# Kernel tuning notes

Measured on AMD Instinct MI355X. Metric: run time of the kernel, lower is better.

## Reference

```python
import jax, jax.numpy as jnp
import numpy as np

N_NODES = 20000
N_EDGES = 320000
N_RELS = 500
EMB = 256
D4 = EMB // 4
B = 32
GAMMA = 12.0
BN_EPS = 1e-5


def _linear(x, W, b):
    return x @ W.T + b


def _bn(x, g, b, m, v):
    # BatchNorm1d in eval mode with running stats
    return (x - m) * jax.lax.rsqrt(v + BN_EPS) * g + b


def _comp_layer(src, dst, h, e, WO, bO, WI, bI, WS, bS, bng, bnb, bnm, bnv):
    # CompGCNLayer: u_sub_e message + per-node mean over in-edges ('ho')
    # and, on the reversed graph, over out-edges ('hi'); nodes with no
    # incident edges get 0 (dgl mean semantics).
    n = h.shape[0]
    ones = jnp.ones(src.shape[0], h.dtype)
    deg_in = jnp.maximum(jax.ops.segment_sum(ones, dst, num_segments=n), 1.0)
    deg_out = jnp.maximum(jax.ops.segment_sum(ones, src, num_segments=n), 1.0)
    ho = jax.ops.segment_sum(h[src] - e, dst, num_segments=n) / deg_in[:, None]
    hi = jax.ops.segment_sum(h[dst] - e, src, num_segments=n) / deg_out[:, None]
    out = (_linear(ho, WO, bO) + _linear(hi, WI, bI) + _linear(h, WS, bS)) / 3.0
    return _bn(out, bng, bnb, bnm, bnv)


def _forward(node_embs, edge_embs, params, src, dst, e_vid, hids, rids, tids,
             is_update_g_embs, is_head_pred):
    (W_O1, b_O1, W_I1, b_I1, W_S1, b_S1, bn1_g, bn1_b, bn1_m, bn1_v, Wr1, br1,
     W_O2, b_O2, W_I2, b_I2, W_S2, b_S2, bn2_g, bn2_b, bn2_m, bn2_v, Wr2, br2) = params
    if is_update_g_embs:
        he = edge_embs[e_vid]                                   # [E, D]
        h1 = jnp.tanh(_comp_layer(src, dst, node_embs, he,
                                  W_O1, b_O1, W_I1, b_I1, W_S1, b_S1,
                                  bn1_g, bn1_b, bn1_m, bn1_v))  # [N, D/4]
        he1 = jnp.tanh(_linear(he, Wr1, br1))                   # [E, D/4]
        hn = jnp.tanh(_comp_layer(src, dst, h1, he1,
                                  W_O2, b_O2, W_I2, b_I2, W_S2, b_S2,
                                  bn2_g, bn2_b, bn2_m, bn2_v))  # [N, D]
    else:
        hn = node_embs
    heads = hn[hids]
    tails = hn[tids]
    rels = _linear(jax.nn.relu(_linear(edge_embs[rids], Wr1, br1)), Wr2, br2)
    b = hids.shape[0]
    n = hn.shape[0]
    # Faithful to torch repeat_interleave indexing in predict():
    # flat element k pairs query row k//C with candidate row k//B.
    cand_idx = (jnp.arange(b)[:, None] * n + jnp.arange(n)[None, :]) // b  # [B, N]
    cand = hn[cand_idx]                                                    # [B, N, D]
    if is_head_pred == 1:
        diff = cand + (rels - tails)[:, None, :]
    else:
        diff = (heads + rels)[:, None, :] - cand
    dist = jnp.sqrt(jnp.sum(diff * diff, axis=-1))  # p = norm = 2
    score = jax.nn.sigmoid(GAMMA - dist)
    return hn, score


def setup_inputs() -> dict:
    key = jax.random.key(0)
    ks = jax.random.split(key, 20)
    w = lambda k, shp: jax.random.normal(k, shp, jnp.float32) * 0.05
    inp = {
        "node_embs": jax.random.normal(ks[0], (N_NODES, EMB), jnp.float32),
        "edge_embs": jax.random.normal(ks[1], (N_RELS, EMB), jnp.float32),
        "W_O1": w(ks[2], (D4, EMB)), "b_O1": jnp.zeros((D4,), jnp.float32),
        "W_I1": w(ks[3], (D4, EMB)), "b_I1": jnp.zeros((D4,), jnp.float32),
        "W_S1": w(ks[4], (D4, EMB)), "b_S1": jnp.zeros((D4,), jnp.float32),
        "bn1_g": jnp.ones((D4,), jnp.float32), "bn1_b": jnp.zeros((D4,), jnp.float32),
        "bn1_m": jnp.zeros((D4,), jnp.float32), "bn1_v": jnp.ones((D4,), jnp.float32),
        "Wr1": w(ks[5], (D4, EMB)), "br1": jnp.zeros((D4,), jnp.float32),
        "W_O2": w(ks[6], (EMB, D4)), "b_O2": jnp.zeros((EMB,), jnp.float32),
        "W_I2": w(ks[7], (EMB, D4)), "b_I2": jnp.zeros((EMB,), jnp.float32),
        "W_S2": w(ks[8], (EMB, D4)), "b_S2": jnp.zeros((EMB,), jnp.float32),
        "bn2_g": jnp.ones((EMB,), jnp.float32), "bn2_b": jnp.zeros((EMB,), jnp.float32),
        "bn2_m": jnp.zeros((EMB,), jnp.float32), "bn2_v": jnp.ones((EMB,), jnp.float32),
        "Wr2": w(ks[9], (EMB, D4)), "br2": jnp.zeros((EMB,), jnp.float32),
        "src": jax.random.randint(ks[10], (N_EDGES,), 0, N_NODES, jnp.int32),
        "dst": jax.random.randint(ks[11], (N_EDGES,), 0, N_NODES, jnp.int32),
        "e_vid": jax.random.randint(ks[12], (N_EDGES,), 0, N_RELS, jnp.int32),
        "hids": jax.random.randint(ks[13], (B,), 0, N_NODES, jnp.int32),
        "rids": jax.random.randint(ks[14], (B,), 0, N_RELS, jnp.int32),
        "tids": jax.random.randint(ks[15], (B,), 0, N_NODES, jnp.int32),
        "is_update_g_embs": 1,
        "is_head_pred": 0,
    }
    return inp


def reference(node_embs, edge_embs,
              W_O1, b_O1, W_I1, b_I1, W_S1, b_S1, bn1_g, bn1_b, bn1_m, bn1_v,
              Wr1, br1,
              W_O2, b_O2, W_I2, b_I2, W_S2, b_S2, bn2_g, bn2_b, bn2_m, bn2_v,
              Wr2, br2,
              src, dst, e_vid, hids, rids, tids,
              is_update_g_embs, is_head_pred):
    params = (W_O1, b_O1, W_I1, b_I1, W_S1, b_S1, bn1_g, bn1_b, bn1_m, bn1_v,
              Wr1, br1,
              W_O2, b_O2, W_I2, b_I2, W_S2, b_S2, bn2_g, bn2_b, bn2_m, bn2_v,
              Wr2, br2)
    return _forward(node_embs, edge_embs, params, src, dst, e_vid,
                    hids, rids, tids, is_update_g_embs, is_head_pred)
```

## Files before the change

kernel.cpp:

```cpp
#include <hip/hip_runtime.h>
#include <math.h>

#define NN 20000
#define NE 320000
#define NR 500
#define EMBD 256
#define D4 64
#define BQ 32
#define TOT (2 * NN)
#define NB 40

#define NBLK_HIST 1250
#define NBLK_BN 448
#define NBLK_K1 (NBLK_HIST + NBLK_BN + 2)

#define NBLK_GC1 939
#define NBLK_GE1 32
#define NBLK_MEGA (NBLK_GC1 + NBLK_GE1 + NBLK_HIST)

typedef __attribute__((ext_vector_type(8))) short bf16x8;
typedef __attribute__((ext_vector_type(4))) float f32x4;

__device__ __forceinline__ unsigned short f2bf(float x)
{
    unsigned int u = __float_as_uint(x);
    unsigned int r = (u + 0x7fffu + ((u >> 16) & 1u)) >> 16;
    return (unsigned short)r;
}

__global__ __launch_bounds__(256) void k_prep(
    const int* __restrict__ src, const int* __restrict__ dst, int* __restrict__ cnt,
    const float* __restrict__ W_O1, const float* __restrict__ W_I1,
    const float* __restrict__ W_S1, const float* __restrict__ Wr1,
    const float* __restrict__ W_O2, const float* __restrict__ W_I2,
    const float* __restrict__ W_S2,
    unsigned short* __restrict__ Bn1, unsigned short* __restrict__ Bn2,
    const float* __restrict__ bO1, const float* __restrict__ bI1,
    const float* __restrict__ bS1,
    const float* __restrict__ g1, const float* __restrict__ bb1,
    const float* __restrict__ m1, const float* __restrict__ v1,
    const float* __restrict__ bO2, const float* __restrict__ bI2,
    const float* __restrict__ bS2,
    const float* __restrict__ g2, const float* __restrict__ bb2,
    const float* __restrict__ m2, const float* __restrict__ v2,
    float* __restrict__ s1, float* __restrict__ t1,
    float* __restrict__ s2, float* __restrict__ t2)
{
    int b = blockIdx.x;
    if (b < NBLK_HIST) {
        int i = b * 256 + threadIdx.x;
        if (i < NE) {
            atomicAdd(&cnt[dst[i]], 1);
            atomicAdd(&cnt[NN + src[i]], 1);
        }
        return;
    }
    b -= NBLK_HIST;
    if (b >= NBLK_BN) {
        int i = (b - NBLK_BN) * 256 + threadIdx.x;
        if (i < 64) {
            float rsg = g1[i] / sqrtf(v1[i] + 1e-5f);
            s1[i] = rsg * (1.f / 3.f);
            t1[i] = ((bO1[i] + bI1[i] + bS1[i]) * (1.f / 3.f) - m1[i]) * rsg + bb1[i];
        } else if (i < 320) {
            int n = i - 64;
            float rsg = g2[n] / sqrtf(v2[n] + 1e-5f);
            s2[n] = rsg * (1.f / 3.f);
            t2[n] = ((bO2[n] + bI2[n] + bS2[n]) * (1.f / 3.f) - m2[n]) * rsg + bb2[n];
        }
        return;
    }
    int id = b * 256 + threadIdx.x;
    if (id < 256 * 256) {
        int n = id >> 8, k = id & 255;
        float v;
        if (n < 64)       v = W_O1[n * 256 + k];
        else if (n < 128) v = W_I1[(n - 64) * 256 + k];
        else if (n < 192) v = W_S1[(n - 128) * 256 + k];
        else              v = Wr1[(n - 192) * 256 + k];
        Bn1[id] = f2bf(v);
    } else {
        int id2 = id - 256 * 256;
        if (id2 < 256 * 192) {
            int n = id2 / 192, k = id2 - n * 192;
            float v;
            if (k < 64)       v = W_O2[n * 64 + k];
            else if (k < 128) v = W_I2[n * 64 + (k - 64)];
            else              v = W_S2[n * 64 + (k - 128)];
            Bn2[id2] = f2bf(v);
        }
    }
}


__global__ __launch_bounds__(256) void k_scanA(const int* __restrict__ cnt,
                                               int* __restrict__ bsum)
{
    __shared__ int lds[256];
    int t = threadIdx.x;
    int base = blockIdx.x * 1024 + t * 4;
    int s = 0;
    if (base + 3 < TOT) {
        int4 v = *(const int4*)(cnt + base);
        s = v.x + v.y + v.z + v.w;
    } else {
        for (int c = 0; c < 4; ++c) { int i = base + c; if (i < TOT) s += cnt[i]; }
    }
    lds[t] = s;
    __syncthreads();
    for (int d = 128; d > 0; d >>= 1) {
        if (t < d) lds[t] += lds[t + d];
        __syncthreads();
    }
    if (t == 0) bsum[blockIdx.x] = lds[0];
}

__global__ __launch_bounds__(64) void k_scanB(int* __restrict__ bsum)
{
    int t = threadIdx.x;
    int v = (t < NB) ? bsum[t] : 0;
#pragma unroll
    for (int d = 1; d < 64; d <<= 1) {
        int u = __shfl_up(v, d, 64);
        if (t >= d) v += u;
    }
    int ex = __shfl_up(v, 1, 64);
    if (t == 0) ex = 0;
    if (t < NB) bsum[t] = ex;
}

__global__ __launch_bounds__(256) void k_scanC(const int* __restrict__ cnt,
                                               const int* __restrict__ bsum,
                                               int* __restrict__ offc,
                                               int* __restrict__ cur)
{
    __shared__ int lds[256];
    int t = threadIdx.x;
    int base = blockIdx.x * 1024 + t * 4;
    int e0 = 0, e1 = 0, e2 = 0, e3 = 0;
    if (base + 3 < TOT) {
        int4 v = *(const int4*)(cnt + base);
        e0 = v.x; e1 = v.y; e2 = v.z; e3 = v.w;
    } else {
        if (base + 0 < TOT) e0 = cnt[base + 0];
        if (base + 1 < TOT) e1 = cnt[base + 1];
        if (base + 2 < TOT) e2 = cnt[base + 2];
        if (base + 3 < TOT) e3 = cnt[base + 3];
    }
    int s = e0 + e1 + e2 + e3;
    lds[t] = s;
    __syncthreads();
    for (int d = 1; d < 256; d <<= 1) {
        int u = (t >= d) ? lds[t - d] : 0;
        __syncthreads();
        lds[t] += u;
        __syncthreads();
    }
    int run = lds[t] - s + bsum[blockIdx.x];
    if (base + 3 < TOT) {
        int4 o = make_int4(run, run + e0, run + e0 + e1, run + e0 + e1 + e2);
        *(int4*)(offc + base) = o;
        *(int4*)(cur + base) = o;
    } else {
        int r = run;
        if (base + 0 < TOT) { offc[base + 0] = r; cur[base + 0] = r; r += e0; }
        if (base + 1 < TOT) { offc[base + 1] = r; cur[base + 1] = r; r += e1; }
        if (base + 2 < TOT) { offc[base + 2] = r; cur[base + 2] = r; r += e2; }
        if (base + 3 < TOT) { offc[base + 3] = r; cur[base + 3] = r; r += e3; }
    }
    if (blockIdx.x == 0 && t == 0) offc[TOT] = 2 * NE;
}

__device__ __forceinline__ void gemm_dev(
    unsigned short* As, unsigned short* Bs,
    const float* __restrict__ A, int M, int K, int lda,
    const unsigned short* __restrict__ Bn,
    float* __restrict__ C, int ldc, int mode,
    const float* __restrict__ sv, const float* __restrict__ tv,
    const float* __restrict__ node_embs, const int* __restrict__ flag,
    int m0, int n0)
{
    const int t = threadIdx.x;
    const int lane = t & 63, wave = t >> 6;
    const int wr = wave >> 1, wc = wave & 1;
    const int lrow = lane & 15, lkg = lane >> 4;

    f32x4 acc[2][2] = {};

    for (int kb = 0; kb < K; kb += 64) {
#pragma unroll
        for (int it = 0; it < 4; ++it) {
            int idx = t + it * 256;
            int kq = idx & 15;
            int row = idx >> 4;
            int gm = m0 + row;
            float4 a = make_float4(0.f, 0.f, 0.f, 0.f);
            if (gm < M) a = *(const float4*)(A + (size_t)gm * lda + kb + 4 * kq);
            unsigned int p0 = (unsigned int)f2bf(a.x) | ((unsigned int)f2bf(a.y) << 16);
            unsigned int p1 = (unsigned int)f2bf(a.z) | ((unsigned int)f2bf(a.w) << 16);
            *(uint2*)&As[row * 72 + 4 * kq] = make_uint2(p0, p1);
        }
#pragma unroll
        for (int it = 0; it < 2; ++it) {
            int idx = t + it * 256;
            int ko = idx & 7;
            int row = idx >> 3;
            uint4 b = *(const uint4*)(Bn + (size_t)(n0 + row) * K + kb + 8 * ko);
            *(uint4*)&Bs[row * 72 + 8 * ko] = b;
        }
        __syncthreads();
#pragma unroll
        for (int ks = 0; ks < 2; ++ks) {
            int k0 = ks * 32 + lkg * 8;
            bf16x8 af0 = *(const bf16x8*)&As[(wr * 32 + lrow) * 72 + k0];
            bf16x8 af1 = *(const bf16x8*)&As[(wr * 32 + 16 + lrow) * 72 + k0];
            bf16x8 bf0 = *(const bf16x8*)&Bs[(wc * 32 + lrow) * 72 + k0];
            bf16x8 bf1 = *(const bf16x8*)&Bs[(wc * 32 + 16 + lrow) * 72 + k0];
            acc[0][0] = __builtin_amdgcn_mfma_f32_16x16x32_bf16(af0, bf0, acc[0][0], 0, 0, 0);
            acc[0][1] = __builtin_amdgcn_mfma_f32_16x16x32_bf16(af0, bf1, acc[0][1], 0, 0, 0);
            acc[1][0] = __builtin_amdgcn_mfma_f32_16x16x32_bf16(af1, bf0, acc[1][0], 0, 0, 0);
            acc[1][1] = __builtin_amdgcn_mfma_f32_16x16x32_bf16(af1, bf1, acc[1][1], 0, 0, 0);
        }
        __syncthreads();
    }

#pragma unroll
    for (int m = 0; m < 2; ++m) {
#pragma unroll
        for (int r = 0; r < 4; ++r) {
            int gm = m0 + wr * 32 + m * 16 + lkg * 4 + r;
            if (gm >= M) continue;
#pragma unroll
            for (int n = 0; n < 2; ++n) {
                int gn = n0 + wc * 32 + n * 16 + lrow;
                float v = acc[m][n][r];
                if (mode == 0) {
                    C[(size_t)gm * ldc + gn] = v;
                } else if (mode == 1) {
                    float val = (gn >= 192) ? tanhf(v + sv[gn - 192]) : v;
                    C[(size_t)gm * ldc + gn] = val;
                } else {
                    float val = tanhf(v * sv[gn] + tv[gn]);
                    if (flag[0] == 0) val = node_embs[(size_t)gm * EMBD + gn];
                    C[(size_t)gm * EMBD + gn] = val;
                }
            }
        }
    }
}

__global__ __launch_bounds__(256) void gemm_mfma(
    const float* __restrict__ A, int M, int K, int lda,
    const unsigned short* __restrict__ Bn,
    float* __restrict__ C, int ldc, int mode,
    const float* __restrict__ sv, const float* __restrict__ tv,
    const float* __restrict__ node_embs, const int* __restrict__ flag)
{
    __shared__ unsigned short As[64 * 72];
    __shared__ unsigned short Bs[64 * 72];
    gemm_dev(As, Bs, A, M, K, lda, Bn, C, ldc, mode, sv, tv, node_embs, flag,
             blockIdx.x * 64, blockIdx.y * 64);
}

__global__ __launch_bounds__(256) void k_mega(
    const float* __restrict__ node_embs, const float* __restrict__ edge_embs,
    const unsigned short* __restrict__ Bn1,
    float* __restrict__ C1, float* __restrict__ E1, const float* __restrict__ br1,
    const int* __restrict__ src, const int* __restrict__ dst,
    const int* __restrict__ evid,
    int* __restrict__ cur, unsigned* __restrict__ R)
{
    __shared__ unsigned short As[64 * 72];
    __shared__ unsigned short Bs[64 * 72];
    int bid = blockIdx.x;
    if (bid < NBLK_GC1) {
        gemm_dev(As, Bs, node_embs, NN, 256, 256, Bn1, C1, 192, 0,
                 nullptr, nullptr, nullptr, nullptr,
                 (bid % 313) * 64, (bid / 313) * 64);
    } else if (bid < NBLK_GC1 + NBLK_GE1) {
        int b2 = bid - NBLK_GC1;
        gemm_dev(As, Bs, edge_embs, NR, 256, 256, Bn1, E1, 256, 1,
                 br1, nullptr, nullptr, nullptr,
                 (b2 % 8) * 64, (b2 / 8) * 64);
    } else {
        int e = (bid - NBLK_GC1 - NBLK_GE1) * 256 + threadIdx.x;
        if (e < NE) {
            int s = src[e], d = dst[e];
            unsigned rv = (unsigned)evid[e] << 15;
            int p = atomicAdd(&cur[d], 1);
            R[p] = (unsigned)s | rv;
            int q = atomicAdd(&cur[NN + s], 1);
            R[q] = (unsigned)d | rv;
        }
    }
}


__device__ __forceinline__ void gather_quad(
    const unsigned* __restrict__ R, int r0, int r1, int g, int q,
    const float* __restrict__ TAB, int ldt, int toff,
    const float* __restrict__ ETAB, int eoff,
    float4& acc)
{
    int lane = g * 16 + q;
    int cnt = r1 - r0;
    for (int base = 0; base < cnt; base += 64) {
        int rem = cnt - base; if (rem > 64) rem = 64;
        unsigned rec = 0u;
        if (lane < rem) rec = R[r0 + base + lane];
        int i = 0;
        for (; 4 * i + 15 < rem; i += 4) {
            unsigned ra = __shfl(rec, 4 * i + g, 64);
            unsigned rb = __shfl(rec, 4 * i + 4 + g, 64);
            unsigned rc = __shfl(rec, 4 * i + 8 + g, 64);
            unsigned rd = __shfl(rec, 4 * i + 12 + g, 64);
            float4 a0 = *(const float4*)(TAB + (size_t)(ra & 0x7FFFu) * ldt + toff + 4 * q);
            float4 e0 = *(const float4*)(ETAB + (size_t)(ra >> 15) * 256 + eoff + 4 * q);
            float4 a1 = *(const float4*)(TAB + (size_t)(rb & 0x7FFFu) * ldt + toff + 4 * q);
            float4 e1 = *(const float4*)(ETAB + (size_t)(rb >> 15) * 256 + eoff + 4 * q);
            float4 a2 = *(const float4*)(TAB + (size_t)(rc & 0x7FFFu) * ldt + toff + 4 * q);
            float4 e2 = *(const float4*)(ETAB + (size_t)(rc >> 15) * 256 + eoff + 4 * q);
            float4 a3 = *(const float4*)(TAB + (size_t)(rd & 0x7FFFu) * ldt + toff + 4 * q);
            float4 e3 = *(const float4*)(ETAB + (size_t)(rd >> 15) * 256 + eoff + 4 * q);
            acc.x += (a0.x - e0.x) + (a1.x - e1.x) + (a2.x - e2.x) + (a3.x - e3.x);
            acc.y += (a0.y - e0.y) + (a1.y - e1.y) + (a2.y - e2.y) + (a3.y - e3.y);
            acc.z += (a0.z - e0.z) + (a1.z - e1.z) + (a2.z - e2.z) + (a3.z - e3.z);
            acc.w += (a0.w - e0.w) + (a1.w - e1.w) + (a2.w - e2.w) + (a3.w - e3.w);
        }
        for (; 4 * i < rem; ++i) {
            int idx = 4 * i + g;
            unsigned rr = __shfl(rec, idx < rem ? idx : 0, 64);
            if (idx < rem) {
                float4 a = *(const float4*)(TAB + (size_t)(rr & 0x7FFFu) * ldt + toff + 4 * q);
                float4 e = *(const float4*)(ETAB + (size_t)(rr >> 15) * 256 + eoff + 4 * q);
                acc.x += a.x - e.x; acc.y += a.y - e.y;
                acc.z += a.z - e.z; acc.w += a.w - e.w;
            }
        }
    }
}

__device__ __forceinline__ void xreduce(float4& v)
{
    v.x += __shfl_xor(v.x, 16, 64); v.y += __shfl_xor(v.y, 16, 64);
    v.z += __shfl_xor(v.z, 16, 64); v.w += __shfl_xor(v.w, 16, 64);
    v.x += __shfl_xor(v.x, 32, 64); v.y += __shfl_xor(v.y, 32, 64);
    v.z += __shfl_xor(v.z, 32, 64); v.w += __shfl_xor(v.w, 32, 64);
}

__global__ __launch_bounds__(256) void k_gather1(
    const int* __restrict__ offc, const unsigned* __restrict__ R,
    const float* __restrict__ C1, const float* __restrict__ E1,
    const float* __restrict__ s1, const float* __restrict__ t1,
    float* __restrict__ A2)
{
    int n = blockIdx.x * 4 + (threadIdx.x >> 6);
    if (n >= NN) return;
    int lane = threadIdx.x & 63, g = lane >> 4, q = lane & 15;
    int b0 = offc[n], b1 = offc[n + 1];
    int c0 = offc[NN + n], c1 = offc[NN + n + 1];
    float di = 1.f / fmaxf((float)(b1 - b0), 1.f);
    float dh = 1.f / fmaxf((float)(c1 - c0), 1.f);
    float4 accO = make_float4(0.f, 0.f, 0.f, 0.f);
    float4 accI = make_float4(0.f, 0.f, 0.f, 0.f);
    gather_quad(R, b0, b1, g, q, C1, 192, 0, E1, 0, accO);
    gather_quad(R, c0, c1, g, q, C1, 192, 64, E1, 64, accI);
    xreduce(accO);
    xreduce(accI);
    if (g == 0) {
        float4 hs = *(const float4*)(C1 + (size_t)n * 192 + 128 + 4 * q);
        float4 sv = *(const float4*)(s1 + 4 * q);
        float4 tv = *(const float4*)(t1 + 4 * q);
        float4 o;
        o.x = tanhf((accO.x * di + accI.x * dh + hs.x) * sv.x + tv.x);
        o.y = tanhf((accO.y * di + accI.y * dh + hs.y) * sv.y + tv.y);
        o.z = tanhf((accO.z * di + accI.z * dh + hs.z) * sv.z + tv.z);
        o.w = tanhf((accO.w * di + accI.w * dh + hs.w) * sv.w + tv.w);
        *(float4*)(A2 + (size_t)n * 192 + 128 + 4 * q) = o;
    }
}

__global__ __launch_bounds__(256) void k_gather2(
    const int* __restrict__ offc, const unsigned* __restrict__ R,
    const float* __restrict__ A2r, const float* __restrict__ E1,
    float* __restrict__ A2w)
{
    int n = blockIdx.x * 4 + (threadIdx.x >> 6);
    if (n >= NN) return;
    int lane = threadIdx.x & 63, g = lane >> 4, q = lane & 15;
    int b0 = offc[n], b1 = offc[n + 1];
    int c0 = offc[NN + n], c1 = offc[NN + n + 1];
    float di = 1.f / fmaxf((float)(b1 - b0), 1.f);
    float dh = 1.f / fmaxf((float)(c1 - c0), 1.f);
    float4 accO = make_float4(0.f, 0.f, 0.f, 0.f);
    float4 accI = make_float4(0.f, 0.f, 0.f, 0.f);
    gather_quad(R, b0, b1, g, q, A2r, 192, 128, E1, 192, accO);
    gather_quad(R, c0, c1, g, q, A2r, 192, 128, E1, 192, accI);
    xreduce(accO);
    xreduce(accI);
    if (g == 0) {
        float4 o0, o1;
        o0.x = accO.x * di; o0.y = accO.y * di; o0.z = accO.z * di; o0.w = accO.w * di;
        o1.x = accI.x * dh; o1.y = accI.y * dh; o1.z = accI.z * dh; o1.w = accI.w * dh;
        *(float4*)(A2w + (size_t)n * 192 + 4 * q) = o0;
        *(float4*)(A2w + (size_t)n * 192 + 64 + 4 * q) = o1;
    }
}

__global__ __launch_bounds__(64) void k_rels(
    const float* __restrict__ edge_embs,
    const float* __restrict__ Wr1, const float* __restrict__ br1,
    const float* __restrict__ Wr2, const float* __restrict__ br2,
    const int* __restrict__ hids, const int* __restrict__ rids, const int* __restrict__ tids,
    const int* __restrict__ is_head, const float* __restrict__ hn,
    float* __restrict__ tvec)
{
    __shared__ float e_s[256];
    __shared__ float m_s[64];
    int b = blockIdx.x, o = threadIdx.x;
    int rid = rids[b];
#pragma unroll
    for (int q = 0; q < 4; ++q) e_s[o + 64 * q] = edge_embs[(size_t)rid * 256 + o + 64 * q];
    __syncthreads();
    float acc = br1[o];
    for (int k = 0; k < 256; ++k) acc = fmaf(e_s[k], Wr1[o * 256 + k], acc);
    m_s[o] = fmaxf(acc, 0.f);
    __syncthreads();
    int ih = is_head[0];
    int nid = ih ? tids[b] : hids[b];
#pragma unroll
    for (int q = 0; q < 4; ++q) {
        int n = o + 64 * q;
        float r = br2[n];
        for (int jj = 0; jj < 64; ++jj) r = fmaf(m_s[jj], Wr2[n * 64 + jj], r);
        float hv = hn[(size_t)nid * 256 + n];
        tvec[b * 256 + n] = ih ? (hv - r) : (hv + r);
    }
}

__global__ __launch_bounds__(256) void k_score(
    const float* __restrict__ hn, const float* __restrict__ tvec,
    float* __restrict__ score)
{
    int p = blockIdx.x * 4 + (threadIdx.x >> 6);
    if (p >= BQ * (NN / BQ)) return;
    int l = threadIdx.x & 63;
    int b = p / (NN / BQ);
    int j = p - b * (NN / BQ);
    int idx = (b * NN + 32 * j) / BQ;
    float ssum = 0.f;
#pragma unroll
    for (int q = 0; q < 4; ++q) {
        float df = hn[(size_t)idx * 256 + l + 64 * q] - tvec[b * 256 + l + 64 * q];
        ssum = fmaf(df, df, ssum);
    }
#pragma unroll
    for (int off = 32; off >= 1; off >>= 1) ssum += __shfl_xor(ssum, off, 64);
    float dist = sqrtf(ssum);
    float sc = 1.f / (1.f + expf(dist - 12.f));
    if (l < 32) score[(size_t)b * NN + 32 * j + l] = sc;
}

extern "C" void kernel_launch(void* const* d_in, const int* in_sizes, int n_in,
                              void* d_out, int out_size, void* d_ws, size_t ws_size,
                              hipStream_t stream)
{
    const float* node_embs = (const float*)d_in[0];
    const float* edge_embs = (const float*)d_in[1];
    const float* W_O1 = (const float*)d_in[2];  const float* b_O1 = (const float*)d_in[3];
    const float* W_I1 = (const float*)d_in[4];  const float* b_I1 = (const float*)d_in[5];
    const float* W_S1 = (const float*)d_in[6];  const float* b_S1 = (const float*)d_in[7];
    const float* bn1_g = (const float*)d_in[8]; const float* bn1_b = (const float*)d_in[9];
    const float* bn1_m = (const float*)d_in[10];const float* bn1_v = (const float*)d_in[11];
    const float* Wr1 = (const float*)d_in[12];  const float* br1 = (const float*)d_in[13];
    const float* W_O2 = (const float*)d_in[14]; const float* b_O2 = (const float*)d_in[15];
    const float* W_I2 = (const float*)d_in[16]; const float* b_I2 = (const float*)d_in[17];
    const float* W_S2 = (const float*)d_in[18]; const float* b_S2 = (const float*)d_in[19];
    const float* bn2_g = (const float*)d_in[20];const float* bn2_b = (const float*)d_in[21];
    const float* bn2_m = (const float*)d_in[22];const float* bn2_v = (const float*)d_in[23];
    const float* Wr2 = (const float*)d_in[24];  const float* br2 = (const float*)d_in[25];
    const int* src = (const int*)d_in[26];
    const int* dst = (const int*)d_in[27];
    const int* evid = (const int*)d_in[28];
    const int* hids = (const int*)d_in[29];
    const int* rids = (const int*)d_in[30];
    const int* tids = (const int*)d_in[31];
    const int* upd = (const int*)d_in[32];
    const int* ihead = (const int*)d_in[33];

    float* ws = (float*)d_ws;
    float* C1   = ws;
    float* A2   = C1 + 3840000;
    float* E1   = A2 + 3840000;
    unsigned short* Bn1 = (unsigned short*)(E1 + 128000);
    unsigned short* Bn2 = Bn1 + 65536;
    float* s1   = (float*)(Bn2 + 49152);
    float* t1   = s1 + 64;
    float* s2   = t1 + 64;
    float* t2   = s2 + 256;
    float* tvec = t2 + 256;

    unsigned* R = (unsigned*)(tvec + 8192);
    int* cnt    = (int*)(R + 2 * NE);
    int* offc   = cnt + TOT;
    int* cur    = offc + TOT + 1;
    int* bsum   = cur + TOT;

    float* hn    = (float*)d_out;
    float* score = hn + (size_t)NN * EMBD;

    hipMemsetAsync(cnt, 0, (size_t)TOT * 4, stream);

    k_prep<<<NBLK_K1, 256, 0, stream>>>(
        src, dst, cnt,
        W_O1, W_I1, W_S1, Wr1, W_O2, W_I2, W_S2, Bn1, Bn2,
        b_O1, b_I1, b_S1, bn1_g, bn1_b, bn1_m, bn1_v,
        b_O2, b_I2, b_S2, bn2_g, bn2_b, bn2_m, bn2_v,
        s1, t1, s2, t2);

    k_scanA<<<NB, 256, 0, stream>>>(cnt, bsum);
    k_scanB<<<1, 64, 0, stream>>>(bsum);
    k_scanC<<<NB, 256, 0, stream>>>(cnt, bsum, offc, cur);

    k_mega<<<NBLK_MEGA, 256, 0, stream>>>(node_embs, edge_embs, Bn1,
                                          C1, E1, br1, src, dst, evid, cur, R);

    k_gather1<<<NN / 4, 256, 0, stream>>>(offc, R, C1, E1, s1, t1, A2);
    k_gather2<<<NN / 4, 256, 0, stream>>>(offc, R, A2, E1, A2);

    gemm_mfma<<<dim3(313, 4), 256, 0, stream>>>(A2, NN, 192, 192, Bn2,
                                                hn, 256, 2, s2, t2, node_embs, upd);

    k_rels<<<BQ, 64, 0, stream>>>(edge_embs, Wr1, br1, Wr2, br2,
                                  hids, rids, tids, ihead, hn, tvec);
    k_score<<<(BQ * (NN / BQ)) / 4, 256, 0, stream>>>(hn, tvec, score);
}
```

Baseline: 172.0 us.

## Store intermediates in bf16, record atomic ranks for CSR fill, hoist rels MLP

Intermediate tables C1, E1 and A2 are now stored as bf16 instead of fp32, which halves the bytes moved by the gather kernels and lets the second GEMM load A tiles directly without converting. The histogram pass keeps the rank returned by each atomicAdd, so the CSR fill can write R at offc plus rank and no longer needs a second round of atomics on a cursor array. The relation MLP moves into the prep kernel as extra blocks, leaving only a small tvec kernel after the final GEMM. The trade-off is extra rounding error from bf16 intermediates and ranks packed into 16 bits, which assumes no node has more than 65535 edges in one direction.

New measurement: 143.2 us. 1.2x faster.

```diff
diff --git a/kernel.cpp b/kernel.cpp
--- a/kernel.cpp
+++ b/kernel.cpp
@@ -12,7 +12,7 @@
 
 #define NBLK_HIST 1250
 #define NBLK_BN 448
-#define NBLK_K1 (NBLK_HIST + NBLK_BN + 2)
+#define NBLK_K1 (NBLK_HIST + NBLK_BN + 2 + BQ)
 
 #define NBLK_GC1 939
 #define NBLK_GE1 32
@@ -28,8 +28,19 @@
     return (unsigned short)r;
 }
 
+__device__ __forceinline__ float4 bf4tof4(uint2 u)
+{
+    float4 r;
+    r.x = __uint_as_float((u.x & 0xFFFFu) << 16);
+    r.y = __uint_as_float(u.x & 0xFFFF0000u);
+    r.z = __uint_as_float((u.y & 0xFFFFu) << 16);
+    r.w = __uint_as_float(u.y & 0xFFFF0000u);
+    return r;
+}
+
 __global__ __launch_bounds__(256) void k_prep(
-    const int* __restrict__ src, const int* __restrict__ dst, int* __restrict__ cnt,
+    const int* __restrict__ src, const int* __restrict__ dst,
+    const int* __restrict__ evid, int* __restrict__ cnt, unsigned* __restrict__ rank2,
     const float* __restrict__ W_O1, const float* __restrict__ W_I1,
     const float* __restrict__ W_S1, const float* __restrict__ Wr1,
     const float* __restrict__ W_O2, const float* __restrict__ W_I2,
@@ -44,20 +55,49 @@
     const float* __restrict__ g2, const float* __restrict__ bb2,
     const float* __restrict__ m2, const float* __restrict__ v2,
     float* __restrict__ s1, float* __restrict__ t1,
-    float* __restrict__ s2, float* __restrict__ t2)
+    float* __restrict__ s2, float* __restrict__ t2,
+    const float* __restrict__ edge_embs,
+    const float* __restrict__ br1, const float* __restrict__ br2,
+    const float* __restrict__ Wr2full, const int* __restrict__ rids,
+    float* __restrict__ rels)
 {
     int b = blockIdx.x;
     if (b < NBLK_HIST) {
         int i = b * 256 + threadIdx.x;
         if (i < NE) {
-            atomicAdd(&cnt[dst[i]], 1);
-            atomicAdd(&cnt[NN + src[i]], 1);
+            int r_in = atomicAdd(&cnt[dst[i]], 1);
+            int r_out = atomicAdd(&cnt[NN + src[i]], 1);
+            rank2[i] = (unsigned)r_in | ((unsigned)r_out << 16);
         }
         return;
     }
     b -= NBLK_HIST;
-    if (b >= NBLK_BN) {
-        int i = (b - NBLK_BN) * 256 + threadIdx.x;
+    if (b < NBLK_BN) {
+        int id = b * 256 + threadIdx.x;
+        if (id < 256 * 256) {
+            int n = id >> 8, k = id & 255;
+            float v;
+            if (n < 64)       v = W_O1[n * 256 + k];
+            else if (n < 128) v = W_I1[(n - 64) * 256 + k];
+            else if (n < 192) v = W_S1[(n - 128) * 256 + k];
+            else              v = Wr1[(n - 192) * 256 + k];
+            Bn1[id] = f2bf(v);
+        } else {
+            int id2 = id - 256 * 256;
+            if (id2 < 256 * 192) {
+                int n = id2 / 192, k = id2 - n * 192;
+                float v;
+                if (k < 64)       v = W_O2[n * 64 + k];
+                else if (k < 128) v = W_I2[n * 64 + (k - 64)];
+                else              v = W_S2[n * 64 + (k - 128)];
+                Bn2[id2] = f2bf(v);
+            }
+        }
+        return;
+    }
+    b -= NBLK_BN;
+    if (b < 2) {
+        int i = b * 256 + threadIdx.x;
         if (i < 64) {
             float rsg = g1[i] / sqrtf(v1[i] + 1e-5f);
             s1[i] = rsg * (1.f / 3.f);
@@ -70,25 +110,22 @@
         }
         return;
     }
-    int id = b * 256 + threadIdx.x;
-    if (id < 256 * 256) {
-        int n = id >> 8, k = id & 255;
-        float v;
-        if (n < 64)       v = W_O1[n * 256 + k];
-        else if (n < 128) v = W_I1[(n - 64) * 256 + k];
-        else if (n < 192) v = W_S1[(n - 128) * 256 + k];
-        else              v = Wr1[(n - 192) * 256 + k];
-        Bn1[id] = f2bf(v);
-    } else {
-        int id2 = id - 256 * 256;
-        if (id2 < 256 * 192) {
-            int n = id2 / 192, k = id2 - n * 192;
-            float v;
-            if (k < 64)       v = W_O2[n * 64 + k];
-            else if (k < 128) v = W_I2[n * 64 + (k - 64)];
-            else              v = W_S2[n * 64 + (k - 128)];
-            Bn2[id2] = f2bf(v);
-        }
+    {
+        __shared__ float e_s[256];
+        __shared__ float m_s[64];
+        int rb = b - 2, o = threadIdx.x;
+        int rid = rids[rb];
+        e_s[o] = edge_embs[(size_t)rid * 256 + o];
+        __syncthreads();
+        if (o < 64) {
+            float acc = br1[o];
+            for (int k = 0; k < 256; ++k) acc = fmaf(e_s[k], Wr1[o * 256 + k], acc);
+            m_s[o] = fmaxf(acc, 0.f);
+        }
+        __syncthreads();
+        float r = br2[o];
+        for (int jj = 0; jj < 64; ++jj) r = fmaf(m_s[jj], Wr2full[o * 64 + jj], r);
+        rels[rb * 256 + o] = r;
     }
 }
 
@@ -131,8 +168,7 @@
 
 __global__ __launch_bounds__(256) void k_scanC(const int* __restrict__ cnt,
                                                const int* __restrict__ bsum,
-                                               int* __restrict__ offc,
-                                               int* __restrict__ cur)
+                                               int* __restrict__ offc)
 {
     __shared__ int lds[256];
     int t = threadIdx.x;
@@ -160,22 +196,21 @@
     if (base + 3 < TOT) {
         int4 o = make_int4(run, run + e0, run + e0 + e1, run + e0 + e1 + e2);
         *(int4*)(offc + base) = o;
-        *(int4*)(cur + base) = o;
     } else {
         int r = run;
-        if (base + 0 < TOT) { offc[base + 0] = r; cur[base + 0] = r; r += e0; }
-        if (base + 1 < TOT) { offc[base + 1] = r; cur[base + 1] = r; r += e1; }
-        if (base + 2 < TOT) { offc[base + 2] = r; cur[base + 2] = r; r += e2; }
-        if (base + 3 < TOT) { offc[base + 3] = r; cur[base + 3] = r; r += e3; }
+        if (base + 0 < TOT) { offc[base + 0] = r; r += e0; }
+        if (base + 1 < TOT) { offc[base + 1] = r; r += e1; }
+        if (base + 2 < TOT) { offc[base + 2] = r; r += e2; }
+        if (base + 3 < TOT) { offc[base + 3] = r; r += e3; }
     }
     if (blockIdx.x == 0 && t == 0) offc[TOT] = 2 * NE;
 }
 
 __device__ __forceinline__ void gemm_dev(
     unsigned short* As, unsigned short* Bs,
-    const float* __restrict__ A, int M, int K, int lda,
+    const void* __restrict__ Av, int aBf16, int M, int K, int lda,
     const unsigned short* __restrict__ Bn,
-    float* __restrict__ C, int ldc, int mode,
+    void* __restrict__ C, int ldc, int mode,
     const float* __restrict__ sv, const float* __restrict__ tv,
     const float* __restrict__ node_embs, const int* __restrict__ flag,
     int m0, int n0)
@@ -188,17 +223,32 @@
     f32x4 acc[2][2] = {};
 
     for (int kb = 0; kb < K; kb += 64) {
-#pragma unroll
-        for (int it = 0; it < 4; ++it) {
-            int idx = t + it * 256;
-            int kq = idx & 15;
-            int row = idx >> 4;
-            int gm = m0 + row;
-            float4 a = make_float4(0.f, 0.f, 0.f, 0.f);
-            if (gm < M) a = *(const float4*)(A + (size_t)gm * lda + kb + 4 * kq);
-            unsigned int p0 = (unsigned int)f2bf(a.x) | ((unsigned int)f2bf(a.y) << 16);
-            unsigned int p1 = (unsigned int)f2bf(a.z) | ((unsigned int)f2bf(a.w) << 16);
-            *(uint2*)&As[row * 72 + 4 * kq] = make_uint2(p0, p1);
+        if (aBf16) {
+            const unsigned short* A = (const unsigned short*)Av;
+#pragma unroll
+            for (int it = 0; it < 2; ++it) {
+                int idx = t + it * 256;
+                int ko = idx & 7;
+                int row = idx >> 3;
+                int gm = m0 + row;
+                uint4 a = make_uint4(0u, 0u, 0u, 0u);
+                if (gm < M) a = *(const uint4*)(A + (size_t)gm * lda + kb + 8 * ko);
+                *(uint4*)&As[row * 72 + 8 * ko] = a;
+            }
+        } else {
+            const float* A = (const float*)Av;
+#pragma unroll
+            for (int it = 0; it < 4; ++it) {
+                int idx = t + it * 256;
+                int kq = idx & 15;
+                int row = idx >> 4;
+                int gm = m0 + row;
+                float4 a = make_float4(0.f, 0.f, 0.f, 0.f);
+                if (gm < M) a = *(const float4*)(A + (size_t)gm * lda + kb + 4 * kq);
+                unsigned int p0 = (unsigned int)f2bf(a.x) | ((unsigned int)f2bf(a.y) << 16);
+                unsigned int p1 = (unsigned int)f2bf(a.z) | ((unsigned int)f2bf(a.w) << 16);
+                *(uint2*)&As[row * 72 + 4 * kq] = make_uint2(p0, p1);
+            }
         }
 #pragma unroll
         for (int it = 0; it < 2; ++it) {
@@ -235,14 +285,14 @@
                 int gn = n0 + wc * 32 + n * 16 + lrow;
                 float v = acc[m][n][r];
                 if (mode == 0) {
-                    C[(size_t)gm * ldc + gn] = v;
+                    ((unsigned short*)C)[(size_t)gm * ldc + gn] = f2bf(v);
                 } else if (mode == 1) {
                     float val = (gn >= 192) ? tanhf(v + sv[gn - 192]) : v;
-                    C[(size_t)gm * ldc + gn] = val;
+                    ((unsigned short*)C)[(size_t)gm * ldc + gn] = f2bf(val);
                 } else {
                     float val = tanhf(v * sv[gn] + tv[gn]);
                     if (flag[0] == 0) val = node_embs[(size_t)gm * EMBD + gn];
-                    C[(size_t)gm * EMBD + gn] = val;
+                    ((float*)C)[(size_t)gm * EMBD + gn] = val;
                 }
             }
         }
@@ -250,36 +300,37 @@
 }
 
 __global__ __launch_bounds__(256) void gemm_mfma(
-    const float* __restrict__ A, int M, int K, int lda,
+    const void* __restrict__ A, int aBf16, int M, int K, int lda,
     const unsigned short* __restrict__ Bn,
-    float* __restrict__ C, int ldc, int mode,
+    void* __restrict__ C, int ldc, int mode,
     const float* __restrict__ sv, const float* __restrict__ tv,
     const float* __restrict__ node_embs, const int* __restrict__ flag)
 {
     __shared__ unsigned short As[64 * 72];
     __shared__ unsigned short Bs[64 * 72];
-    gemm_dev(As, Bs, A, M, K, lda, Bn, C, ldc, mode, sv, tv, node_embs, flag,
+    gemm_dev(As, Bs, A, aBf16, M, K, lda, Bn, C, ldc, mode, sv, tv, node_embs, flag,
              blockIdx.x * 64, blockIdx.y * 64);
 }
 
 __global__ __launch_bounds__(256) void k_mega(
     const float* __restrict__ node_embs, const float* __restrict__ edge_embs,
     const unsigned short* __restrict__ Bn1,
-    float* __restrict__ C1, float* __restrict__ E1, const float* __restrict__ br1,
+    unsigned short* __restrict__ C1b, unsigned short* __restrict__ E1b,
+    const float* __restrict__ br1,
     const int* __restrict__ src, const int* __restrict__ dst,
-    const int* __restrict__ evid,
-    int* __restrict__ cur, unsigned* __restrict__ R)
+    const int* __restrict__ evid, const unsigned* __restrict__ rank2,
+    const int* __restrict__ offc, unsigned* __restrict__ R)
 {
     __shared__ unsigned short As[64 * 72];
     __shared__ unsigned short Bs[64 * 72];
     int bid = blockIdx.x;
     if (bid < NBLK_GC1) {
-        gemm_dev(As, Bs, node_embs, NN, 256, 256, Bn1, C1, 192, 0,
+        gemm_dev(As, Bs, node_embs, 0, NN, 256, 256, Bn1, C1b, 192, 0,
                  nullptr, nullptr, nullptr, nullptr,
                  (bid % 313) * 64, (bid / 313) * 64);
     } else if (bid < NBLK_GC1 + NBLK_GE1) {
         int b2 = bid - NBLK_GC1;
-        gemm_dev(As, Bs, edge_embs, NR, 256, 256, Bn1, E1, 256, 1,
+        gemm_dev(As, Bs, edge_embs, 0, NR, 256, 256, Bn1, E1b, 256, 1,
                  br1, nullptr, nullptr, nullptr,
                  (b2 % 8) * 64, (b2 / 8) * 64);
     } else {
@@ -287,10 +338,9 @@
         if (e < NE) {
             int s = src[e], d = dst[e];
             unsigned rv = (unsigned)evid[e] << 15;
-            int p = atomicAdd(&cur[d], 1);
-            R[p] = (unsigned)s | rv;
-            int q = atomicAdd(&cur[NN + s], 1);
-            R[q] = (unsigned)d | rv;
+            unsigned rk = rank2[e];
+            R[offc[d] + (rk & 0xFFFFu)] = (unsigned)s | rv;
+            R[offc[NN + s] + (rk >> 16)] = (unsigned)d | rv;
         }
     }
 }
@@ -298,8 +348,8 @@
 
 __device__ __forceinline__ void gather_quad(
     const unsigned* __restrict__ R, int r0, int r1, int g, int q,
-    const float* __restrict__ TAB, int ldt, int toff,
-    const float* __restrict__ ETAB, int eoff,
+    const unsigned short* __restrict__ TAB, int ldt, int toff,
+    const unsigned short* __restrict__ ETAB, int eoff,
     float4& acc)
 {
     int lane = g * 16 + q;
@@ -314,14 +364,18 @@
             unsigned rb = __shfl(rec, 4 * i + 4 + g, 64);
             unsigned rc = __shfl(rec, 4 * i + 8 + g, 64);
             unsigned rd = __shfl(rec, 4 * i + 12 + g, 64);
-            float4 a0 = *(const float4*)(TAB + (size_t)(ra & 0x7FFFu) * ldt + toff + 4 * q);
-            float4 e0 = *(const float4*)(ETAB + (size_t)(ra >> 15) * 256 + eoff + 4 * q);
-            float4 a1 = *(const float4*)(TAB + (size_t)(rb & 0x7FFFu) * ldt + toff + 4 * q);
-            float4 e1 = *(const float4*)(ETAB + (size_t)(rb >> 15) * 256 + eoff + 4 * q);
-            float4 a2 = *(const float4*)(TAB + (size_t)(rc & 0x7FFFu) * ldt + toff + 4 * q);
-            float4 e2 = *(const float4*)(ETAB + (size_t)(rc >> 15) * 256 + eoff + 4 * q);
-            float4 a3 = *(const float4*)(TAB + (size_t)(rd & 0x7FFFu) * ldt + toff + 4 * q);
-            float4 e3 = *(const float4*)(ETAB + (size_t)(rd >> 15) * 256 + eoff + 4 * q);
+            uint2 ua0 = *(const uint2*)(TAB + (size_t)(ra & 0x7FFFu) * ldt + toff + 4 * q);
+            uint2 ue0 = *(const uint2*)(ETAB + (size_t)(ra >> 15) * 256 + eoff + 4 * q);
+            uint2 ua1 = *(const uint2*)(TAB + (size_t)(rb & 0x7FFFu) * ldt + toff + 4 * q);
+            uint2 ue1 = *(const uint2*)(ETAB + (size_t)(rb >> 15) * 256 + eoff + 4 * q);
+            uint2 ua2 = *(const uint2*)(TAB + (size_t)(rc & 0x7FFFu) * ldt + toff + 4 * q);
+            uint2 ue2 = *(const uint2*)(ETAB + (size_t)(rc >> 15) * 256 + eoff + 4 * q);
+            uint2 ua3 = *(const uint2*)(TAB + (size_t)(rd & 0x7FFFu) * ldt + toff + 4 * q);
+            uint2 ue3 = *(const uint2*)(ETAB + (size_t)(rd >> 15) * 256 + eoff + 4 * q);
+            float4 a0 = bf4tof4(ua0), e0 = bf4tof4(ue0);
+            float4 a1 = bf4tof4(ua1), e1 = bf4tof4(ue1);
+            float4 a2 = bf4tof4(ua2), e2 = bf4tof4(ue2);
+            float4 a3 = bf4tof4(ua3), e3 = bf4tof4(ue3);
             acc.x += (a0.x - e0.x) + (a1.x - e1.x) + (a2.x - e2.x) + (a3.x - e3.x);
             acc.y += (a0.y - e0.y) + (a1.y - e1.y) + (a2.y - e2.y) + (a3.y - e3.y);
             acc.z += (a0.z - e0.z) + (a1.z - e1.z) + (a2.z - e2.z) + (a3.z - e3.z);
@@ -331,8 +385,9 @@
             int idx = 4 * i + g;
             unsigned rr = __shfl(rec, idx < rem ? idx : 0, 64);
             if (idx < rem) {
-                float4 a = *(const float4*)(TAB + (size_t)(rr & 0x7FFFu) * ldt + toff + 4 * q);
-                float4 e = *(const float4*)(ETAB + (size_t)(rr >> 15) * 256 + eoff + 4 * q);
+                uint2 ua = *(const uint2*)(TAB + (size_t)(rr & 0x7FFFu) * ldt + toff + 4 * q);
+                uint2 ue = *(const uint2*)(ETAB + (size_t)(rr >> 15) * 256 + eoff + 4 * q);
+                float4 a = bf4tof4(ua), e = bf4tof4(ue);
                 acc.x += a.x - e.x; acc.y += a.y - e.y;
                 acc.z += a.z - e.z; acc.w += a.w - e.w;
             }
@@ -348,11 +403,17 @@
     v.z += __shfl_xor(v.z, 32, 64); v.w += __shfl_xor(v.w, 32, 64);
 }
 
+__device__ __forceinline__ uint2 packbf4(float4 o)
+{
+    return make_uint2((unsigned)f2bf(o.x) | ((unsigned)f2bf(o.y) << 16),
+                      (unsigned)f2bf(o.z) | ((unsigned)f2bf(o.w) << 16));
+}
+
 __global__ __launch_bounds__(256) void k_gather1(
     const int* __restrict__ offc, const unsigned* __restrict__ R,
-    const float* __restrict__ C1, const float* __restrict__ E1,
+    const unsigned short* __restrict__ C1b, const unsigned short* __restrict__ E1b,
     const float* __restrict__ s1, const float* __restrict__ t1,
-    float* __restrict__ A2)
+    unsigned short* __restrict__ A2b)
 {
     int n = blockIdx.x * 4 + (threadIdx.x >> 6);
     if (n >= NN) return;
@@ -363,12 +424,12 @@
     float dh = 1.f / fmaxf((float)(c1 - c0), 1.f);
     float4 accO = make_float4(0.f, 0.f, 0.f, 0.f);
     float4 accI = make_float4(0.f, 0.f, 0.f, 0.f);
-    gather_quad(R, b0, b1, g, q, C1, 192, 0, E1, 0, accO);
-    gather_quad(R, c0, c1, g, q, C1, 192, 64, E1, 64, accI);
+    gather_quad(R, b0, b1, g, q, C1b, 192, 0, E1b, 0, accO);
+    gather_quad(R, c0, c1, g, q, C1b, 192, 64, E1b, 64, accI);
     xreduce(accO);
     xreduce(accI);
     if (g == 0) {
-        float4 hs = *(const float4*)(C1 + (size_t)n * 192 + 128 + 4 * q);
+        float4 hs = bf4tof4(*(const uint2*)(C1b + (size_t)n * 192 + 128 + 4 * q));
         float4 sv = *(const float4*)(s1 + 4 * q);
         float4 tv = *(const float4*)(t1 + 4 * q);
         float4 o;
@@ -376,14 +437,14 @@
         o.y = tanhf((accO.y * di + accI.y * dh + hs.y) * sv.y + tv.y);
         o.z = tanhf((accO.z * di + accI.z * dh + hs.z) * sv.z + tv.z);
         o.w = tanhf((accO.w * di + accI.w * dh + hs.w) * sv.w + tv.w);
-        *(float4*)(A2 + (size_t)n * 192 + 128 + 4 * q) = o;
+        *(uint2*)(A2b + (size_t)n * 192 + 128 + 4 * q) = packbf4(o);
     }
 }
 
 __global__ __launch_bounds__(256) void k_gather2(
     const int* __restrict__ offc, const unsigned* __restrict__ R,
-    const float* __restrict__ A2r, const float* __restrict__ E1,
-    float* __restrict__ A2w)
+    const unsigned short* __restrict__ A2r, const unsigned short* __restrict__ E1b,
+    unsigned short* __restrict__ A2w)
 {
     int n = blockIdx.x * 4 + (threadIdx.x >> 6);
     if (n >= NN) return;
@@ -394,48 +455,30 @@
     float dh = 1.f / fmaxf((float)(c1 - c0), 1.f);
     float4 accO = make_float4(0.f, 0.f, 0.f, 0.f);
     float4 accI = make_float4(0.f, 0.f, 0.f, 0.f);
-    gather_quad(R, b0, b1, g, q, A2r, 192, 128, E1, 192, accO);
-    gather_quad(R, c0, c1, g, q, A2r, 192, 128, E1, 192, accI);
+    gather_quad(R, b0, b1, g, q, A2r, 192, 128, E1b, 192, accO);
+    gather_quad(R, c0, c1, g, q, A2r, 192, 128, E1b, 192, accI);
     xreduce(accO);
     xreduce(accI);
     if (g == 0) {
         float4 o0, o1;
         o0.x = accO.x * di; o0.y = accO.y * di; o0.z = accO.z * di; o0.w = accO.w * di;
         o1.x = accI.x * dh; o1.y = accI.y * dh; o1.z = accI.z * dh; o1.w = accI.w * dh;
-        *(float4*)(A2w + (size_t)n * 192 + 4 * q) = o0;
-        *(float4*)(A2w + (size_t)n * 192 + 64 + 4 * q) = o1;
-    }
-}
-
-__global__ __launch_bounds__(64) void k_rels(
-    const float* __restrict__ edge_embs,
-    const float* __restrict__ Wr1, const float* __restrict__ br1,
-    const float* __restrict__ Wr2, const float* __restrict__ br2,
-    const int* __restrict__ hids, const int* __restrict__ rids, const int* __restrict__ tids,
-    const int* __restrict__ is_head, const float* __restrict__ hn,
-    float* __restrict__ tvec)
-{
-    __shared__ float e_s[256];
-    __shared__ float m_s[64];
+        *(uint2*)(A2w + (size_t)n * 192 + 4 * q) = packbf4(o0);
+        *(uint2*)(A2w + (size_t)n * 192 + 64 + 4 * q) = packbf4(o1);
+    }
+}
+
+__global__ __launch_bounds__(256) void k_tvec(
+    const float* __restrict__ rels, const float* __restrict__ hn,
+    const int* __restrict__ hids, const int* __restrict__ tids,
+    const int* __restrict__ is_head, float* __restrict__ tvec)
+{
     int b = blockIdx.x, o = threadIdx.x;
-    int rid = rids[b];
-#pragma unroll
-    for (int q = 0; q < 4; ++q) e_s[o + 64 * q] = edge_embs[(size_t)rid * 256 + o + 64 * q];
-    __syncthreads();
-    float acc = br1[o];
-    for (int k = 0; k < 256; ++k) acc = fmaf(e_s[k], Wr1[o * 256 + k], acc);
-    m_s[o] = fmaxf(acc, 0.f);
-    __syncthreads();
     int ih = is_head[0];
     int nid = ih ? tids[b] : hids[b];
-#pragma unroll
-    for (int q = 0; q < 4; ++q) {
-        int n = o + 64 * q;
-        float r = br2[n];
-        for (int jj = 0; jj < 64; ++jj) r = fmaf(m_s[jj], Wr2[n * 64 + jj], r);
-        float hv = hn[(size_t)nid * 256 + n];
-        tvec[b * 256 + n] = ih ? (hv - r) : (hv + r);
-    }
+    float r = rels[b * 256 + o];
+    float hv = hn[(size_t)nid * 256 + o];
+    tvec[b * 256 + o] = ih ? (hv - r) : (hv + r);
 }
 
 __global__ __launch_bounds__(256) void k_score(
@@ -488,23 +531,24 @@
     const int* upd = (const int*)d_in[32];
     const int* ihead = (const int*)d_in[33];
 
-    float* ws = (float*)d_ws;
-    float* C1   = ws;
-    float* A2   = C1 + 3840000;
-    float* E1   = A2 + 3840000;
-    unsigned short* Bn1 = (unsigned short*)(E1 + 128000);
+    unsigned short* C1b = (unsigned short*)d_ws;
+    unsigned short* A2b = C1b + 3840000;
+    unsigned short* E1b = A2b + 3840000;
+    unsigned short* Bn1 = E1b + 128000;
     unsigned short* Bn2 = Bn1 + 65536;
+
     float* s1   = (float*)(Bn2 + 49152);
     float* t1   = s1 + 64;
     float* s2   = t1 + 64;
     float* t2   = s2 + 256;
-    float* tvec = t2 + 256;
-
-    unsigned* R = (unsigned*)(tvec + 8192);
-    int* cnt    = (int*)(R + 2 * NE);
+    float* rels = t2 + 256;
+    float* tvec = rels + 8192;
+
+    unsigned* R     = (unsigned*)(tvec + 8192);
+    unsigned* rank2 = R + 2 * NE;
+    int* cnt    = (int*)(rank2 + NE);
     int* offc   = cnt + TOT;
-    int* cur    = offc + TOT + 1;
-    int* bsum   = cur + TOT;
+    int* bsum   = offc + TOT + 1;
 
     float* hn    = (float*)d_out;
     float* score = hn + (size_t)NN * EMBD;
@@ -512,26 +556,26 @@
     hipMemsetAsync(cnt, 0, (size_t)TOT * 4, stream);
 
     k_prep<<<NBLK_K1, 256, 0, stream>>>(
-        src, dst, cnt,
+        src, dst, evid, cnt, rank2,
         W_O1, W_I1, W_S1, Wr1, W_O2, W_I2, W_S2, Bn1, Bn2,
         b_O1, b_I1, b_S1, bn1_g, bn1_b, bn1_m, bn1_v,
         b_O2, b_I2, b_S2, bn2_g, bn2_b, bn2_m, bn2_v,
-        s1, t1, s2, t2);
+        s1, t1, s2, t2,
+        edge_embs, br1, br2, Wr2, rids, rels);
 
     k_scanA<<<NB, 256, 0, stream>>>(cnt, bsum);
     k_scanB<<<1, 64, 0, stream>>>(bsum);
-    k_scanC<<<NB, 256, 0, stream>>>(cnt, bsum, offc, cur);
+    k_scanC<<<NB, 256, 0, stream>>>(cnt, bsum, offc);
 
     k_mega<<<NBLK_MEGA, 256, 0, stream>>>(node_embs, edge_embs, Bn1,
-                                          C1, E1, br1, src, dst, evid, cur, R);
-
-    k_gather1<<<NN / 4, 256, 0, stream>>>(offc, R, C1, E1, s1, t1, A2);
-    k_gather2<<<NN / 4, 256, 0, stream>>>(offc, R, A2, E1, A2);
-
-    gemm_mfma<<<dim3(313, 4), 256, 0, stream>>>(A2, NN, 192, 192, Bn2,
+                                          C1b, E1b, br1, src, dst, evid, rank2, offc, R);
+
+    k_gather1<<<NN / 4, 256, 0, stream>>>(offc, R, C1b, E1b, s1, t1, A2b);
+    k_gather2<<<NN / 4, 256, 0, stream>>>(offc, R, A2b, E1b, A2b);
+
+    gemm_mfma<<<dim3(313, 4), 256, 0, stream>>>(A2b, 1, NN, 192, 192, Bn2,
                                                 hn, 256, 2, s2, t2, node_embs, upd);
 
-    k_rels<<<BQ, 64, 0, stream>>>(edge_embs, Wr1, br1, Wr2, br2,
-                                  hids, rids, tids, ihead, hn, tvec);
+    k_tvec<<<BQ, 256, 0, stream>>>(rels, hn, hids, tids, ihead, tvec);
     k_score<<<(BQ * (NN / BQ)) / 4, 256, 0, stream>>>(hn, tvec, score);
 }
```
